# Optimization experiments

Measured on AMD Instinct MI355X. Metric: run time of the kernel, lower is better.

The kernel has to match this reference:

```python
import jax, jax.numpy as jnp
import numpy as np

B, N, M, D = 4096, 39, 32, 32   # batch, fields, embed_dim, product_layer_dim
F = 1_000_000                   # features_dim (sparse vocab)
H = [400, 400, 400]             # hidden layer sizes
BN_EPS = 1e-3                   # keras BatchNormalization default epsilon


def setup_inputs() -> dict:
    key = jax.random.key(0)
    ks = jax.random.split(key, 32)
    inp = {
        "feature_index": jax.random.randint(ks[0], (B, N), 0, F),
        "feature_value": jax.random.normal(ks[1], (B, N), dtype=jnp.float32),
        # keras Embedding default 'uniform' initializer: U(-0.05, 0.05)
        "emb_table": jax.random.uniform(ks[2], (F, M), minval=-0.05, maxval=0.05, dtype=jnp.float32),
        "lin_w": jax.random.normal(ks[3], (D, N, M), dtype=jnp.float32) * 0.05,
        "quad_w": jax.random.normal(ks[4], (D, N), dtype=jnp.float32) * 0.1,
    }
    # MLP: input is concat(l_z, l_p) -> 2*D wide
    dims = [2 * D] + H
    k = 5
    for i in range(len(H)):
        fan_in, fan_out = dims[i], dims[i + 1]
        scale = (2.0 / (fan_in + fan_out)) ** 0.5
        inp[f"W{i}"] = jax.random.normal(ks[k], (fan_in, fan_out), dtype=jnp.float32) * scale; k += 1
        inp[f"b{i}"] = jnp.zeros((fan_out,), jnp.float32)
        inp[f"g{i}"] = jnp.ones((fan_out,), jnp.float32)    # BN gamma
        inp[f"be{i}"] = jnp.zeros((fan_out,), jnp.float32)  # BN beta
        inp[f"rm{i}"] = jnp.zeros((fan_out,), jnp.float32)  # BN moving mean
        inp[f"rv{i}"] = jnp.ones((fan_out,), jnp.float32)   # BN moving var
    inp["Wout"] = jax.random.normal(ks[k], (H[-1], 1), dtype=jnp.float32) * 0.05
    inp["bout"] = jnp.zeros((1,), jnp.float32)
    return inp


def _forward(feature_index, emb_table, lin_w, quad_w, layer_params, Wout, bout):
    e = emb_table[feature_index]                          # (B, N, M) embedding lookup
    l_z = jnp.einsum('bnm,dnm->bd', e, lin_w)             # linear signal
    theta = jnp.einsum('bnm,dn->bdnm', e, quad_w)         # IPNN quadratic signal
    l_p = jnp.einsum('bdnm,bdnm->bd', theta, theta)       # sum of squares over (n, m)
    x = jnp.concatenate([l_z, l_p], axis=1)               # (B, 2D)
    for (W, b, g, be, rm, rv) in layer_params:
        x = x @ W + b
        x = (x - rm) * jax.lax.rsqrt(rv + BN_EPS) * g + be  # BN (inference stats)
        x = jax.nn.relu(x)
    return jax.nn.sigmoid(x @ Wout + bout)                # (B, 1)


def reference(feature_index, feature_value, emb_table, lin_w, quad_w,
              W0, b0, g0, be0, rm0, rv0,
              W1, b1, g1, be1, rm1, rv1,
              W2, b2, g2, be2, rm2, rv2,
              Wout, bout):
    # feature_value is accepted by the original call() but never used; dropout disabled (eval).
    layer_params = [
        (W0, b0, g0, be0, rm0, rv0),
        (W1, b1, g1, be1, rm1, rv1),
        (W2, b2, g2, be2, rm2, rv2),
    ]
    return _forward(feature_index, emb_table, lin_w, quad_w, layer_params, Wout, bout)
```

## Files before the change

### kernel.cpp

```cpp
#include <hip/hip_runtime.h>
#include <hip/hip_bf16.h>
#include <math.h>

#define TB 4096
#define TN 39
#define TM 32
#define TD 32
#define TH 400
#define BN_EPS 1e-3f

#define KT0 2
#define KTH 13

typedef __attribute__((ext_vector_type(8))) short bf16x8;
typedef __attribute__((ext_vector_type(4))) float f32x4;

__device__ __forceinline__ ushort bf16_rn(float x) {
    __hip_bfloat16 h = __float2bfloat16(x);
    union { __hip_bfloat16 b; ushort u; } c; c.b = h; return c.u;
}
__device__ __forceinline__ void split2(float x, ushort& hi, ushort& lo) {
    unsigned xb = __float_as_uint(x);
    unsigned hb = xb & 0xFFFF0000u;
    hi = (ushort)(hb >> 16);
    lo = bf16_rn(x - __uint_as_float(hb));
}

__device__ __forceinline__ size_t panel_idx(int p, int k, int KT) {
    int lane_ = (p & 15) + 16 * ((k >> 2) & 3);
    int j_    = (k & 3) + 4 * ((k >> 4) & 1);
    return (((size_t)((p >> 4) * KT + (k >> 5)) * 64) + lane_) * 8 + j_;
}

__global__ __launch_bounds__(256) void fused_front_kernel(
    const int*   __restrict__ fidx,
    const float* __restrict__ emb,
    const float* __restrict__ lin_w,
    const float* __restrict__ quad_w,
    const float* __restrict__ W0, const float* __restrict__ W1, const float* __restrict__ W2,
    const float* __restrict__ b0_, const float* __restrict__ g0_, const float* __restrict__ be0_,
    const float* __restrict__ rm0_, const float* __restrict__ rv0_,
    const float* __restrict__ b1_, const float* __restrict__ g1_, const float* __restrict__ be1_,
    const float* __restrict__ rm1_, const float* __restrict__ rv1_,
    const float* __restrict__ b2_, const float* __restrict__ g2_, const float* __restrict__ be2_,
    const float* __restrict__ rm2_, const float* __restrict__ rv2_,
    ushort* __restrict__ A0h, ushort* __restrict__ A0l,
    ushort* __restrict__ B0h, ushort* __restrict__ B0l,
    ushort* __restrict__ B1h, ushort* __restrict__ B1l,
    ushort* __restrict__ B2h, ushort* __restrict__ B2l,
    float* __restrict__ AC)
{
    if (blockIdx.x >= TB / 4) {
        int tid = (blockIdx.x - TB / 4) * 256 + threadIdx.x;
        const int NW0 = 64 * 112, NW = 416 * 112;
        if (tid < NW0 + 2 * NW) {
            const float* W; ushort *Ph, *Pl; int k, n4, K, KT;
            if (tid < NW0) {
                W = W0; Ph = B0h; Pl = B0l; k = tid / 112; n4 = tid % 112; K = 64; KT = KT0;
            } else if (tid < NW0 + NW) {
                int u = tid - NW0;
                W = W1; Ph = B1h; Pl = B1l; k = u / 112; n4 = u % 112; K = TH; KT = KTH;
            } else {
                int u = tid - NW0 - NW;
                W = W2; Ph = B2h; Pl = B2l; k = u / 112; n4 = u % 112; K = TH; KT = KTH;
            }
            int n0 = n4 * 4;
            float4 w = make_float4(0.f, 0.f, 0.f, 0.f);
            if (k < K && n0 < TH)
                w = *(const float4*)&W[(size_t)k * TH + n0];
            float vals[4] = {w.x, w.y, w.z, w.w};
            #pragma unroll
            for (int i = 0; i < 4; ++i) {
                ushort hi, lo; split2(vals[i], hi, lo);
                size_t idx = panel_idx(n0 + i, k, KT);
                Ph[idx] = hi; Pl[idx] = lo;
            }
        } else if (tid < NW0 + 2 * NW + 3 * 448) {
            int u = tid - NW0 - 2 * NW;
            int layer = u / 448, h = u % 448;
            const float *gp, *bep, *rmp, *rvp, *bp;
            if (layer == 0)      { gp = g0_; bep = be0_; rmp = rm0_; rvp = rv0_; bp = b0_; }
            else if (layer == 1) { gp = g1_; bep = be1_; rmp = rm1_; rvp = rv1_; bp = b1_; }
            else                 { gp = g2_; bep = be2_; rmp = rm2_; rvp = rv2_; bp = b2_; }
            float aj = 0.f, cj = 0.f;
            if (h < TH) {
                aj = gp[h] * rsqrtf(rvp[h] + BN_EPS);
                cj = (bp[h] - rmp[h]) * aj + bep[h];
            }
            AC[layer * 896 + h] = aj;
            AC[layer * 896 + 448 + h] = cj;
        }
        return;
    }

    constexpr int R = 4;
    __shared__ float e_s[R][TN * TM];
    __shared__ int   idx_s[R][TN];
    __shared__ float s_s[R][TN];

    const int t  = threadIdx.x;
    const int b0 = blockIdx.x * R;

    if (t < R * TN) {
        int r = t / TN, n = t - r * TN;
        idx_s[r][n] = fidx[(b0 + r) * TN + n];
    }
    __syncthreads();

    for (int r = 0; r < R; ++r) {
        for (int k4 = t; k4 < TN * TM / 4; k4 += 256) {
            int n = k4 >> 3;
            long long base = (long long)idx_s[r][n] * TM + ((k4 & 7) << 2);
            *(float4*)&e_s[r][k4 * 4] = *(const float4*)&emb[base];
        }
    }
    __syncthreads();

    {
        const int d = t >> 3, j = t & 7;
        float acc[R] = {0.f, 0.f, 0.f, 0.f};
        const float* lw_base = lin_w + d * (TN * TM);
        #pragma unroll 4
        for (int i = 0; i < TN; ++i) {
            float4 lw = *(const float4*)&lw_base[i * 32 + j * 4];
            #pragma unroll
            for (int r = 0; r < R; ++r) {
                float4 e4 = *(const float4*)&e_s[r][i * 32 + j * 4];
                acc[r] = fmaf(lw.x, e4.x, acc[r]);
                acc[r] = fmaf(lw.y, e4.y, acc[r]);
                acc[r] = fmaf(lw.z, e4.z, acc[r]);
                acc[r] = fmaf(lw.w, e4.w, acc[r]);
            }
        }
        #pragma unroll
        for (int off = 1; off < 8; off <<= 1)
            #pragma unroll
            for (int r = 0; r < R; ++r)
                acc[r] += __shfl_xor(acc[r], off);
        if (j == 0) {
            #pragma unroll
            for (int r = 0; r < R; ++r) {
                ushort hi, lo; split2(acc[r], hi, lo);
                size_t idx = panel_idx(b0 + r, d, KT0);
                A0h[idx] = hi; A0l[idx] = lo;
            }
        }
    }

    {
        int r = t >> 6, lane = t & 63;
        if (lane < TN) {
            float s = 0.f;
            #pragma unroll
            for (int mm = 0; mm < TM; ++mm) {
                float v = e_s[r][lane * TM + ((lane + mm) & 31)];
                s = fmaf(v, v, s);
            }
            s_s[r][lane] = s;
        }
    }
    __syncthreads();

    if (t < R * TD) {
        int r = t >> 5, d = t & 31;
        float accv = 0.f;
        for (int n = 0; n < TN; ++n) {
            float q = quad_w[d * TN + n];
            accv = fmaf(s_s[r][n], q * q, accv);
        }
        ushort hi, lo; split2(accv, hi, lo);
        size_t idx = panel_idx(b0 + r, TD + d, KT0);
        A0h[idx] = hi; A0l[idx] = lo;
    }
}

template <int KT, int OUTMODE>
__global__ __launch_bounds__(128) void gemm_layer_v5(
    const ushort* __restrict__ Ah, const ushort* __restrict__ Al,
    const ushort* __restrict__ Bh, const ushort* __restrict__ Bl,
    const float* __restrict__ ACl,
    ushort* __restrict__ Nh, ushort* __restrict__ Nl,
    const float* __restrict__ Wout,
    float* __restrict__ P)
{
    const int lane = threadIdx.x & 63;
    const int nsel = threadIdx.x >> 6;
    const int bm = blockIdx.x;
    const int bn = blockIdx.y;

    f32x4 acc[2][2];
    #pragma unroll
    for (int m = 0; m < 2; ++m)
        #pragma unroll
        for (int n = 0; n < 2; ++n)
            acc[m][n] = (f32x4){0.f, 0.f, 0.f, 0.f};

    const size_t lo8 = (size_t)lane * 8;
    const ushort* pAh = Ah + (size_t)(bm * 2) * KT * 512 + lo8;
    const ushort* pAl = Al + (size_t)(bm * 2) * KT * 512 + lo8;
    const ushort* pBh = Bh + (size_t)(bn * 4 + nsel * 2) * KT * 512 + lo8;
    const ushort* pBl = Bl + (size_t)(bn * 4 + nsel * 2) * KT * 512 + lo8;

    #pragma unroll 2
    for (int kt = 0; kt < KT; ++kt) {
        bf16x8 ah[2], al[2], bh[2], bl[2];
        #pragma unroll
        for (int m = 0; m < 2; ++m) {
            ah[m] = *(const bf16x8*)(pAh + (size_t)(m * KT + kt) * 512);
            al[m] = *(const bf16x8*)(pAl + (size_t)(m * KT + kt) * 512);
        }
        #pragma unroll
        for (int n = 0; n < 2; ++n) {
            bh[n] = *(const bf16x8*)(pBh + (size_t)(n * KT + kt) * 512);
            bl[n] = *(const bf16x8*)(pBl + (size_t)(n * KT + kt) * 512);
        }
        #pragma unroll
        for (int m = 0; m < 2; ++m)
            #pragma unroll
            for (int n = 0; n < 2; ++n) {
                acc[m][n] = __builtin_amdgcn_mfma_f32_16x16x32_bf16(ah[m], bh[n], acc[m][n], 0, 0, 0);
                acc[m][n] = __builtin_amdgcn_mfma_f32_16x16x32_bf16(ah[m], bl[n], acc[m][n], 0, 0, 0);
                acc[m][n] = __builtin_amdgcn_mfma_f32_16x16x32_bf16(al[m], bh[n], acc[m][n], 0, 0, 0);
            }
    }

    const int col = lane & 15, rq = (lane >> 4) << 2;

    if constexpr (OUTMODE == 0) {
        __shared__ float ysm[32][68];
        #pragma unroll
        for (int m = 0; m < 2; ++m)
            #pragma unroll
            for (int n = 0; n < 2; ++n) {
                int h = bn * 64 + (nsel * 2 + n) * 16 + col;
                float aj = ACl[h], cj = ACl[448 + h];
                #pragma unroll
                for (int r = 0; r < 4; ++r)
                    ysm[m * 16 + rq + r][(nsel * 2 + n) * 16 + col] =
                        fmaxf(fmaf(acc[m][n][r], aj, cj), 0.f);
            }
        __syncthreads();

        const int ck = nsel;
        const int kt32 = bn * 2 + ck;
        if (kt32 < KTH) {
            #pragma unroll
            for (int mtl = 0; mtl < 2; ++mtl) {
                int row_l = mtl * 16 + (lane & 15);
                int kb = ck * 32 + rq;
                float4 v0 = *(const float4*)&ysm[row_l][kb];
                float4 v1 = *(const float4*)&ysm[row_l][kb + 16];
                ushort h_[8], l_[8];
                split2(v0.x, h_[0], l_[0]); split2(v0.y, h_[1], l_[1]);
                split2(v0.z, h_[2], l_[2]); split2(v0.w, h_[3], l_[3]);
                split2(v1.x, h_[4], l_[4]); split2(v1.y, h_[5], l_[5]);
                split2(v1.z, h_[6], l_[6]); split2(v1.w, h_[7], l_[7]);
                uint4 H, L;
                H.x = (uint)h_[0] | ((uint)h_[1] << 16);
                H.y = (uint)h_[2] | ((uint)h_[3] << 16);
                H.z = (uint)h_[4] | ((uint)h_[5] << 16);
                H.w = (uint)h_[6] | ((uint)h_[7] << 16);
                L.x = (uint)l_[0] | ((uint)l_[1] << 16);
                L.y = (uint)l_[2] | ((uint)l_[3] << 16);
                L.z = (uint)l_[4] | ((uint)l_[5] << 16);
                L.w = (uint)l_[6] | ((uint)l_[7] << 16);
                size_t base = (((size_t)(bm * 2 + mtl) * KTH + kt32) * 64 + lane) * 8;
                *(uint4*)(Nh + base) = H;
                *(uint4*)(Nl + base) = L;
            }
        }
    } else {
        float partial[2][4] = {{0.f,0.f,0.f,0.f},{0.f,0.f,0.f,0.f}};
        #pragma unroll
        for (int m = 0; m < 2; ++m)
            #pragma unroll
            for (int n = 0; n < 2; ++n) {
                int h = bn * 64 + (nsel * 2 + n) * 16 + col;
                float aj = ACl[h], cj = ACl[448 + h];
                float wv = (h < TH) ? Wout[h] : 0.f;
                #pragma unroll
                for (int r = 0; r < 4; ++r) {
                    float y = fmaxf(fmaf(acc[m][n][r], aj, cj), 0.f);
                    partial[m][r] = fmaf(y, wv, partial[m][r]);
                }
            }
        #pragma unroll
        for (int off = 1; off < 16; off <<= 1)
            #pragma unroll
            for (int m = 0; m < 2; ++m)
                #pragma unroll
                for (int r = 0; r < 4; ++r)
                    partial[m][r] += __shfl_xor(partial[m][r], off);
        if (col == 0) {
            #pragma unroll
            for (int m = 0; m < 2; ++m)
                #pragma unroll
                for (int r = 0; r < 4; ++r)
                    P[(size_t)(bm * 32 + m * 16 + rq + r) * 16 + bn * 2 + nsel] =
                        partial[m][r];
        }
    }
}

__global__ __launch_bounds__(256) void fin_kernel(
    const float* __restrict__ P, const float* __restrict__ bout,
    float* __restrict__ out)
{
    int row = blockIdx.x * 256 + threadIdx.x;
    const float* p = P + (size_t)row * 16;
    float s = bout[0];
    #pragma unroll
    for (int i = 0; i < 14; ++i) s += p[i];
    out[row] = 1.f / (1.f + expf(-s));
}

extern "C" void kernel_launch(void* const* d_in, const int* in_sizes, int n_in,
                              void* d_out, int out_size, void* d_ws, size_t ws_size,
                              hipStream_t stream) {
    const int*   fidx   = (const int*)  d_in[0];
    const float* emb    = (const float*)d_in[2];
    const float* lin_w  = (const float*)d_in[3];
    const float* quad_w = (const float*)d_in[4];

    const float* W0  = (const float*)d_in[5];
    const float* b0  = (const float*)d_in[6];
    const float* g0  = (const float*)d_in[7];
    const float* be0 = (const float*)d_in[8];
    const float* rm0 = (const float*)d_in[9];
    const float* rv0 = (const float*)d_in[10];

    const float* W1  = (const float*)d_in[11];
    const float* b1  = (const float*)d_in[12];
    const float* g1  = (const float*)d_in[13];
    const float* be1 = (const float*)d_in[14];
    const float* rm1 = (const float*)d_in[15];
    const float* rv1 = (const float*)d_in[16];

    const float* W2  = (const float*)d_in[17];
    const float* b2  = (const float*)d_in[18];
    const float* g2  = (const float*)d_in[19];
    const float* be2 = (const float*)d_in[20];
    const float* rm2 = (const float*)d_in[21];
    const float* rv2 = (const float*)d_in[22];

    const float* Wout = (const float*)d_in[23];
    const float* bout = (const float*)d_in[24];

    const size_t SZ_A0 = (size_t)256 * KT0 * 512;
    const size_t SZ_A  = (size_t)256 * KTH * 512;
    const size_t SZ_B0 = (size_t)28  * KT0 * 512;
    const size_t SZ_B  = (size_t)28  * KTH * 512;

    ushort* p = (ushort*)d_ws;
    ushort *A0h = p; p += SZ_A0; ushort *A0l = p; p += SZ_A0;
    ushort *A1h = p; p += SZ_A;  ushort *A1l = p; p += SZ_A;
    ushort *A2h = p; p += SZ_A;  ushort *A2l = p; p += SZ_A;
    ushort *B0h = p; p += SZ_B0; ushort *B0l = p; p += SZ_B0;
    ushort *B1h = p; p += SZ_B;  ushort *B1l = p; p += SZ_B;
    ushort *B2h = p; p += SZ_B;  ushort *B2l = p; p += SZ_B;
    float*  AC  = (float*)p;
    float*  Pst = AC + 3 * 896;

    fused_front_kernel<<<TB / 4 + 398, 256, 0, stream>>>(
        fidx, emb, lin_w, quad_w, W0, W1, W2,
        b0, g0, be0, rm0, rv0,
        b1, g1, be1, rm1, rv1,
        b2, g2, be2, rm2, rv2,
        A0h, A0l, B0h, B0l, B1h, B1l, B2h, B2l, AC);

    dim3 ggrid(128, 7);
    gemm_layer_v5<KT0, 0><<<ggrid, 128, 0, stream>>>(
        A0h, A0l, B0h, B0l, AC + 0, A1h, A1l, nullptr, nullptr);
    gemm_layer_v5<KTH, 0><<<ggrid, 128, 0, stream>>>(
        A1h, A1l, B1h, B1l, AC + 896, A2h, A2l, nullptr, nullptr);
    gemm_layer_v5<KTH, 1><<<ggrid, 128, 0, stream>>>(
        A2h, A2l, B2h, B2l, AC + 1792, nullptr, nullptr, Wout, Pst);

    fin_kernel<<<TB / 256, 256, 0, stream>>>(Pst, bout, (float*)d_out);
}
```

Before: 53.98 us.

## Double GEMM block M-tile to 4 waves with XCD-aware block remapping

Each GEMM block now runs 4 waves covering 64 rows by 64 columns instead of 2 waves covering 32 rows, so B panels are shared by twice as many rows per block and the grid halves to 448 blocks. The 1D block index is remapped so that consecutive blocks on the same XCD share B column tiles, aiming to improve L2 locality. The final reduction kernel switches to float4 loads. Risks are fewer blocks to fill the 256 CUs and a larger shared-memory footprint per block.

```diff
diff --git a/kernel.cpp b/kernel.cpp
--- a/kernel.cpp
+++ b/kernel.cpp
@@ -175,7 +175,7 @@
 }
 
 template <int KT, int OUTMODE>
-__global__ __launch_bounds__(128) void gemm_layer_v5(
+__global__ __launch_bounds__(256) void gemm_layer_v6(
     const ushort* __restrict__ Ah, const ushort* __restrict__ Al,
     const ushort* __restrict__ Bh, const ushort* __restrict__ Bl,
     const float* __restrict__ ACl,
@@ -184,9 +184,15 @@
     float* __restrict__ P)
 {
     const int lane = threadIdx.x & 63;
-    const int nsel = threadIdx.x >> 6;
-    const int bm = blockIdx.x;
-    const int bn = blockIdx.y;
+    const int wv   = threadIdx.x >> 6;
+    const int msel = wv >> 1;
+    const int nsel = wv & 1;
+
+    const int orig = blockIdx.x;
+    const int xcd  = orig & 7;
+    const int slot = orig >> 3;
+    const int bm   = (slot & 7) * 8 + xcd;
+    const int bn   = slot >> 3;
 
     f32x4 acc[2][2];
     #pragma unroll
@@ -196,8 +202,8 @@
             acc[m][n] = (f32x4){0.f, 0.f, 0.f, 0.f};
 
     const size_t lo8 = (size_t)lane * 8;
-    const ushort* pAh = Ah + (size_t)(bm * 2) * KT * 512 + lo8;
-    const ushort* pAl = Al + (size_t)(bm * 2) * KT * 512 + lo8;
+    const ushort* pAh = Ah + (size_t)(bm * 4 + msel * 2) * KT * 512 + lo8;
+    const ushort* pAl = Al + (size_t)(bm * 4 + msel * 2) * KT * 512 + lo8;
     const ushort* pBh = Bh + (size_t)(bn * 4 + nsel * 2) * KT * 512 + lo8;
     const ushort* pBl = Bl + (size_t)(bn * 4 + nsel * 2) * KT * 512 + lo8;
 
@@ -227,7 +233,7 @@
     const int col = lane & 15, rq = (lane >> 4) << 2;
 
     if constexpr (OUTMODE == 0) {
-        __shared__ float ysm[32][68];
+        __shared__ float ysm[64][68];
         #pragma unroll
         for (int m = 0; m < 2; ++m)
             #pragma unroll
@@ -236,16 +242,17 @@
                 float aj = ACl[h], cj = ACl[448 + h];
                 #pragma unroll
                 for (int r = 0; r < 4; ++r)
-                    ysm[m * 16 + rq + r][(nsel * 2 + n) * 16 + col] =
+                    ysm[msel * 32 + m * 16 + rq + r][(nsel * 2 + n) * 16 + col] =
                         fmaxf(fmaf(acc[m][n][r], aj, cj), 0.f);
             }
         __syncthreads();
 
-        const int ck = nsel;
+        const int ck = wv & 1;
         const int kt32 = bn * 2 + ck;
         if (kt32 < KTH) {
             #pragma unroll
-            for (int mtl = 0; mtl < 2; ++mtl) {
+            for (int mi = 0; mi < 2; ++mi) {
+                int mtl = (wv >> 1) * 2 + mi;
                 int row_l = mtl * 16 + (lane & 15);
                 int kb = ck * 32 + rq;
                 float4 v0 = *(const float4*)&ysm[row_l][kb];
@@ -264,7 +271,7 @@
                 L.y = (uint)l_[2] | ((uint)l_[3] << 16);
                 L.z = (uint)l_[4] | ((uint)l_[5] << 16);
                 L.w = (uint)l_[6] | ((uint)l_[7] << 16);
-                size_t base = (((size_t)(bm * 2 + mtl) * KTH + kt32) * 64 + lane) * 8;
+                size_t base = (((size_t)(bm * 4 + mtl) * KTH + kt32) * 64 + lane) * 8;
                 *(uint4*)(Nh + base) = H;
                 *(uint4*)(Nl + base) = L;
             }
@@ -277,11 +284,11 @@
             for (int n = 0; n < 2; ++n) {
                 int h = bn * 64 + (nsel * 2 + n) * 16 + col;
                 float aj = ACl[h], cj = ACl[448 + h];
-                float wv = (h < TH) ? Wout[h] : 0.f;
+                float wv_ = (h < TH) ? Wout[h] : 0.f;
                 #pragma unroll
                 for (int r = 0; r < 4; ++r) {
                     float y = fmaxf(fmaf(acc[m][n][r], aj, cj), 0.f);
-                    partial[m][r] = fmaf(y, wv, partial[m][r]);
+                    partial[m][r] = fmaf(y, wv_, partial[m][r]);
                 }
             }
         #pragma unroll
@@ -296,8 +303,8 @@
             for (int m = 0; m < 2; ++m)
                 #pragma unroll
                 for (int r = 0; r < 4; ++r)
-                    P[(size_t)(bm * 32 + m * 16 + rq + r) * 16 + bn * 2 + nsel] =
-                        partial[m][r];
+                    P[(size_t)(bm * 64 + msel * 32 + m * 16 + rq + r) * 16
+                      + bn * 2 + nsel] = partial[m][r];
         }
     }
 }
@@ -307,10 +314,13 @@
     float* __restrict__ out)
 {
     int row = blockIdx.x * 256 + threadIdx.x;
-    const float* p = P + (size_t)row * 16;
-    float s = bout[0];
-    #pragma unroll
-    for (int i = 0; i < 14; ++i) s += p[i];
+    const float4* p = (const float4*)(P + (size_t)row * 16);
+    float4 p0 = p[0], p1 = p[1], p2 = p[2], p3 = p[3];
+    float s = bout[0]
+            + p0.x + p0.y + p0.z + p0.w
+            + p1.x + p1.y + p1.z + p1.w
+            + p2.x + p2.y + p2.z + p2.w
+            + p3.x + p3.y;
     out[row] = 1.f / (1.f + expf(-s));
 }
 
@@ -368,12 +378,11 @@
         b2, g2, be2, rm2, rv2,
         A0h, A0l, B0h, B0l, B1h, B1l, B2h, B2l, AC);
 
-    dim3 ggrid(128, 7);
-    gemm_layer_v5<KT0, 0><<<ggrid, 128, 0, stream>>>(
+    gemm_layer_v6<KT0, 0><<<448, 256, 0, stream>>>(
         A0h, A0l, B0h, B0l, AC + 0, A1h, A1l, nullptr, nullptr);
-    gemm_layer_v5<KTH, 0><<<ggrid, 128, 0, stream>>>(
+    gemm_layer_v6<KTH, 0><<<448, 256, 0, stream>>>(
         A1h, A1l, B1h, B1l, AC + 896, A2h, A2l, nullptr, nullptr);
-    gemm_layer_v5<KTH, 1><<<ggrid, 128, 0, stream>>>(
+    gemm_layer_v6<KTH, 1><<<448, 256, 0, stream>>>(
         A2h, A2l, B2h, B2l, AC + 1792, nullptr, nullptr, Wout, Pst);
 
     fin_kernel<<<TB / 256, 256, 0, stream>>>(Pst, bout, (float*)d_out);
```

New measurement: 51.42 us. -4.7%, faster.
